# Kernel tuning notes

Measured on AMD Instinct MI355X. Metric: run time of the kernel, lower is better.

## Reference

```python
import jax, jax.numpy as jnp
import numpy as np

KNN_K = 5  # nearest neighbors for local density
PATCH_GRID = 14  # hard-coded p1=p2=14 in rearrange


def _tokens(x):
    # b c (p1 h) (p2 w) -> b (p1 p2) (h w c)
    B, C, H, W = x.shape
    P = PATCH_GRID
    h, w = H // P, W // P
    t = x.reshape(B, C, P, h, P, w).transpose(0, 2, 4, 3, 5, 1)
    return t.reshape(B, P * P, h * w * C)


def _forward(x, len_keep):
    t = _tokens(x)
    B, N, Cf = t.shape
    # pairwise Euclidean distance (torch.cdist) scaled by sqrt(C)
    sq = jnp.sum(t * t, axis=-1)  # [B, N]
    d2 = sq[:, :, None] + sq[:, None, :] - 2.0 * jnp.einsum('bnc,bmc->bnm', t, t)
    dist = jnp.sqrt(jnp.maximum(d2, 0.0)) / jnp.sqrt(jnp.asarray(Cf, dist_dtype := t.dtype))
    # k-NN local density
    neg_vals, _ = jax.lax.top_k(-dist, KNN_K)  # k smallest distances
    dist_nearest = -neg_vals  # [B, N, k]
    density = jnp.exp(-jnp.mean(dist_nearest ** 2, axis=-1))  # [B, N]
    kd = jax.random.fold_in(jax.random.key(1), 0)
    density = density + jax.random.uniform(kd, density.shape, dtype=density.dtype) * 1e-6
    # distance to nearest higher-density point (masked min reduction)
    maskf = (density[:, None, :] > density[:, :, None]).astype(dist.dtype)  # [B, N, N]
    dist_max = jnp.max(dist.reshape(B, -1), axis=-1)[:, None, None]
    dmin = jnp.min(dist * maskf + dist_max * (1.0 - maskf), axis=-1)  # [B, N]
    score = dmin * density
    # pick cluster centers: top len_keep scores
    _, index_down = jax.lax.top_k(score, len_keep)  # [B, K]
    # assign each token to nearest center
    dm_down = jnp.take_along_axis(dist, index_down[:, :, None], axis=1)  # [B, K, N]
    idx_cluster = jnp.argmin(dm_down, axis=1)  # [B, N]
    # force centers to their own cluster id
    idx_cluster = idx_cluster.at[jnp.arange(B)[:, None], index_down].set(
        jnp.arange(len_keep)[None, :])
    # per-cluster counts (every cluster id 0..K-1 present since centers self-assign)
    counts = jnp.sum(jax.nn.one_hot(idx_cluster, len_keep, dtype=jnp.int32), axis=1)  # [B, K]
    idx_counts = jnp.cumsum(counts, axis=-1)
    # pick one representative token per cluster via noisy sort
    kn = jax.random.fold_in(jax.random.key(1), 1)
    noise = jax.random.uniform(kn, (B, N), dtype=dist.dtype)
    order = jnp.argsort(idx_cluster.astype(dist.dtype) + noise, axis=-1)
    idx = jnp.take_along_axis(order, idx_counts - 1, axis=1)  # [B, K]
    return idx


def setup_inputs() -> dict:
    key = jax.random.key(0)
    x = jax.random.normal(key, (256, 3, 224, 224), dtype=jnp.float32)
    return {"x": x, "len_keep": 49}


def reference(x, len_keep):
    return _forward(x, len_keep)
```

## Files before the change

### kernel.cpp

```cpp
#include <hip/hip_runtime.h>
#include <stdint.h>

#define NTOK 196
#define KCL 49
#define IMG 224
#define IMG2 (224*224)
#define KB 64
#define LDP 68

typedef double f64x4 __attribute__((ext_vector_type(4)));

__host__ __device__ __forceinline__ void tf2x32(uint32_t k0, uint32_t k1,
    uint32_t x0, uint32_t x1, uint32_t* o0, uint32_t* o1) {
  uint32_t ks2 = k0 ^ k1 ^ 0x1BD11BDAu;
#define TFR(r) { x0 += x1; x1 = (x1 << r) | (x1 >> (32 - r)); x1 ^= x0; }
  x0 += k0; x1 += k1;
  TFR(13) TFR(15) TFR(26) TFR(6)
  x0 += k1; x1 += ks2 + 1u;
  TFR(17) TFR(29) TFR(16) TFR(24)
  x0 += ks2; x1 += k0 + 2u;
  TFR(13) TFR(15) TFR(26) TFR(6)
  x0 += k0; x1 += k1 + 3u;
  TFR(17) TFR(29) TFR(16) TFR(24)
  x0 += k1; x1 += ks2 + 4u;
  TFR(13) TFR(15) TFR(26) TFR(6)
  x0 += ks2; x1 += k0 + 5u;
#undef TFR
  *o0 = x0; *o1 = x1;
}

__device__ __forceinline__ float jax_uniform(uint32_t k0, uint32_t k1, uint32_t j) {
  uint32_t o0, o1;
  tf2x32(k0, k1, 0u, j, &o0, &o1);
  uint32_t bits = o0 ^ o1;
  return __uint_as_float((bits >> 9) | 0x3f800000u) - 1.0f;
}

__global__ void __launch_bounds__(256) k_sq(const float* __restrict__ x,
                                            double* __restrict__ sq, int B) {
  int wave = blockIdx.x * 4 + (threadIdx.x >> 6);
  int lane = threadIdx.x & 63;
  if (wave >= B * NTOK) return;
  int b = wave / NTOK, n = wave % NTOK;
  int p1 = n / 14, p2 = n % 14;
  const float* xb = x + (size_t)b * 3 * IMG2;
  int rowbase = (p1 * 16) * IMG + p2 * 16;
  double acc = 0.0;
#pragma unroll
  for (int q = 0; q < 12; ++q) {
    int f = lane + q * 64;
    int c = f >> 8, h = (f >> 4) & 15, w = f & 15;
    float v = xb[c * IMG2 + rowbase + h * IMG + w];
    acc += (double)v * (double)v;
  }
#pragma unroll
  for (int off = 32; off; off >>= 1) acc += __shfl_down(acc, off);
  if (lane == 0) sq[wave] = acc;
}

__global__ void __launch_bounds__(256) k_dist_mfma(const float* __restrict__ x,
    const double* __restrict__ sq, double* __restrict__ dist,
    unsigned long long* __restrict__ dmax) {
  int bid = blockIdx.x;
  int xcd = bid & 7;
  int s = bid >> 3;
  int b = xcd + 8 * (s / 28);
  int t = s % 28;
  int ti = 0, rem = t, rl = 7;
  while (rem >= rl) { rem -= rl; rl--; ti++; }
  int tj = ti + rem;
  int n0b = ti * 32, m0b = tj * 32;
  int tid = threadIdx.x;

  __shared__ __align__(16) float As[32][LDP];
  __shared__ __align__(16) float Bs[32][LDP];
  __shared__ int rbN[32], rbM[32];
  __shared__ double prsh[3];
  __shared__ int okf;

  if (tid < 32) {
    int n = n0b + tid; n = n < NTOK ? n : NTOK - 1;
    rbN[tid] = (n / 14) * 16 * IMG + (n % 14) * 16;
  } else if (tid < 64) {
    int m = m0b + (tid - 32); m = m < NTOK ? m : NTOK - 1;
    rbM[tid - 32] = (m / 14) * 16 * IMG + (m % 14) * 16;
  }
  __syncthreads();

  const float* xb = x + (size_t)b * 3 * IMG2;
  int srow = tid >> 3;
  int sfo  = (tid & 7) * 8;
  int rN = rbN[srow], rM = rbM[srow];
  int lane = tid & 63;
  int wid  = tid >> 6;
  int wi = wid >> 1, wj = wid & 1;
  int aq = lane >> 4;
  const float* Ap = &As[0][0];
  const float* Bp = &Bs[0][0];
  int abase = (wi * 16 + (lane & 15)) * LDP + aq;
  int bbase = (wj * 16 + (lane & 15)) * LDP + aq;

#define LOADT(d0,d1,d2,d3,kc) { int f0 = (kc) + sfo;                         \
    int c_ = f0 >> 8, h_ = (f0 >> 4) & 15, w_ = f0 & 15;                     \
    const float* p_ = xb + c_ * IMG2 + h_ * IMG + w_;                        \
    d0 = *(const float4*)(p_ + rN); d1 = *(const float4*)(p_ + rN + 4);      \
    d2 = *(const float4*)(p_ + rM); d3 = *(const float4*)(p_ + rM + 4); }

  f64x4 acc = {0.0, 0.0, 0.0, 0.0};
  f64x4 acc0 = {0.0, 0.0, 0.0, 0.0};
  float4 ca0, ca1, cb0, cb1;
  LOADT(ca0, ca1, cb0, cb1, 0)

#pragma unroll
  for (int tt = 0; tt < 12; ++tt) {
    __syncthreads();
    *(float4*)&As[srow][sfo]     = ca0;
    *(float4*)&As[srow][sfo + 4] = ca1;
    *(float4*)&Bs[srow][sfo]     = cb0;
    *(float4*)&Bs[srow][sfo + 4] = cb1;
    __syncthreads();
    float4 na0, na1, nb0, nb1;
    if (tt < 11) LOADT(na0, na1, nb0, nb1, (tt + 1) * KB)
#pragma unroll
    for (int k = 0; k < KB; k += 4) {
      double av = (double)Ap[abase + k];
      double bv = (double)Bp[bbase + k];
      acc = __builtin_amdgcn_mfma_f64_16x16x4f64(av, bv, acc, 0, 0, 0);
    }
    if (tt == 0) {
      if (wid == 0) {
        double q0 = (double)As[0][lane] * (double)Bs[0][lane];
        double q1 = (double)As[1][lane] * (double)Bs[0][lane];
        double q2 = (double)As[4][lane] * (double)Bs[0][lane];
#pragma unroll
        for (int off = 32; off; off >>= 1) {
          q0 += __shfl_down(q0, off);
          q1 += __shfl_down(q1, off);
          q2 += __shfl_down(q2, off);
        }
        if (lane == 0) { prsh[0] = q0; prsh[1] = q1; prsh[2] = q2; }
      }
      acc0 = acc;
    }
    ca0 = na0; ca1 = na1; cb0 = nb0; cb1 = nb1;
  }
#undef LOADT

  if (tid == 0) {
    double tol = 1e-9 * (1.0 + fabs(prsh[0]));
    int ok0  = fabs(prsh[0] - acc0[0]) <= tol;
    int okP1 = ok0 && (fabs(prsh[1] - acc0[1]) <= tol);
    int okP2 = ok0 && (fabs(prsh[2] - acc0[1]) <= tol);
    okf = okP1 ? 1 : (okP2 ? 2 : 0);
  }
  __syncthreads();
  int mode = okf;

  double (*Dt)[33] = (double(*)[33])(&As[0][0]);

  if (mode) {
#pragma unroll
    for (int i = 0; i < 4; ++i) {
      int lr = (mode == 1) ? (aq * 4 + i) : (aq + 4 * i);
      Dt[wi * 16 + lr][wj * 16 + (lane & 15)] = acc[i];
    }
  } else {
    double s00 = 0, s01 = 0, s10 = 0, s11 = 0;
    int ty2 = tid >> 4, tx2 = tid & 15;
    for (int kc = 0; kc < 768; kc += KB) {
      int f0 = kc + sfo;
      int c_ = f0 >> 8, h_ = (f0 >> 4) & 15, w_ = f0 & 15;
      const float* p_ = xb + c_ * IMG2 + h_ * IMG + w_;
      float4 la0 = *(const float4*)(p_ + rN), la1 = *(const float4*)(p_ + rN + 4);
      float4 lb0 = *(const float4*)(p_ + rM), lb1 = *(const float4*)(p_ + rM + 4);
      __syncthreads();
      *(float4*)&As[srow][sfo]     = la0;
      *(float4*)&As[srow][sfo + 4] = la1;
      *(float4*)&Bs[srow][sfo]     = lb0;
      *(float4*)&Bs[srow][sfo + 4] = lb1;
      __syncthreads();
      for (int j = 0; j < KB; ++j) {
        double a0 = (double)As[ty2][j], a1 = (double)As[ty2 + 16][j];
        double b0 = (double)Bs[tx2][j], b1 = (double)Bs[tx2 + 16][j];
        s00 += a0 * b0; s01 += a0 * b1; s10 += a1 * b0; s11 += a1 * b1;
      }
    }
    __syncthreads();
    Dt[ty2][tx2] = s00;       Dt[ty2][tx2 + 16] = s01;
    Dt[ty2 + 16][tx2] = s10;  Dt[ty2 + 16][tx2 + 16] = s11;
  }
  __syncthreads();

  const double* sqb = sq + b * NTOK;
  const double SQ768 = sqrt(768.0);
  int lr2 = tid >> 3, lc0 = (tid & 7) * 4;
  double dv[4];
  double lmax = 0.0;
#pragma unroll
  for (int j = 0; j < 4; ++j) {
    int n = n0b + lr2, m = m0b + lc0 + j;
    int nn = n < NTOK ? n : NTOK - 1, mm = m < NTOK ? m : NTOK - 1;
    double d2 = sqb[nn] + sqb[mm] - 2.0 * Dt[lr2][lc0 + j];
    double d = sqrt(d2 > 0.0 ? d2 : 0.0) / SQ768;
    dv[j] = d;
    lmax = lmax > d ? lmax : d;
  }
#pragma unroll
  for (int j = 0; j < 4; ++j) Dt[lr2][lc0 + j] = dv[j];
  double* red = (double*)(&Bs[0][0]);
  red[tid] = lmax;
  __syncthreads();
  for (int st = 128; st; st >>= 1) {
    if (tid < st) { double o = red[tid + st]; if (o > red[tid]) red[tid] = o; }
    __syncthreads();
  }
  if (tid == 0) atomicMax(&dmax[b], (unsigned long long)__double_as_longlong(red[0]));

  double* Db = dist + (size_t)b * NTOK * NTOK;
  {
    int n = n0b + lr2, m0 = m0b + lc0;
    if (n < NTOK && m0 < NTOK) {
      if (m0 + 3 < NTOK) {
        f64x4 v = {dv[0], dv[1], dv[2], dv[3]};
        *(f64x4*)(Db + (size_t)n * NTOK + m0) = v;
      } else {
#pragma unroll
        for (int j = 0; j < 4; ++j)
          if (m0 + j < NTOK) Db[(size_t)n * NTOK + m0 + j] = dv[j];
      }
    }
  }
  if (ti != tj) {
    int m = m0b + lr2, n0 = n0b + lc0;
    if (m < NTOK && n0 < NTOK) {
      if (n0 + 3 < NTOK) {
        f64x4 v = {Dt[lc0][lr2], Dt[lc0 + 1][lr2], Dt[lc0 + 2][lr2], Dt[lc0 + 3][lr2]};
        *(f64x4*)(Db + (size_t)m * NTOK + n0) = v;
      } else {
#pragma unroll
        for (int j = 0; j < 4; ++j)
          if (n0 + j < NTOK) Db[(size_t)m * NTOK + n0 + j] = Dt[lc0 + j][lr2];
      }
    }
  }
}

#define INS5(n0_,n1_,n2_,n3_,n4_,v_) {                                        \
  if ((v_) < n4_) { n4_ = (v_);                                               \
    if (n4_ < n3_) { double w_ = n3_; n3_ = n4_; n4_ = w_;                    \
      if (n3_ < n2_) { w_ = n2_; n2_ = n3_; n3_ = w_;                         \
        if (n2_ < n1_) { w_ = n1_; n1_ = n2_; n2_ = w_;                       \
          if (n1_ < n0_) { w_ = n0_; n0_ = n1_; n1_ = w_; } } } } } }

__global__ void __launch_bounds__(512) k_cluster2(const double* __restrict__ dist,
    const unsigned long long* __restrict__ dmax, int* __restrict__ out,
    uint32_t kd0, uint32_t kd1, uint32_t kn0, uint32_t kn1, int B) {
  int b = blockIdx.x;
  int tid = threadIdx.x;
  int lane = tid & 63, wid = tid >> 6;
  const double* Db = dist + (size_t)b * NTOK * NTOK;
  __shared__ double nbsh[NTOK * 5];
  __shared__ double dens[NTOK];
  __shared__ double score[NTOK];
  __shared__ int center[KCL];
  __shared__ short center_of[NTOK];
  __shared__ unsigned long long bkey[KCL];
  double dmaxv = __longlong_as_double((long long)dmax[b]);

  int t = (tid < NTOK) ? tid : tid - NTOK;
  int half = (tid < NTOK) ? 0 : 1;
  bool act = tid < 2 * NTOK;
  int m0 = half ? 98 : 0;

  double pa0 = 1e300, pa1 = 1e300, pa2 = 1e300, pa3 = 1e300, pa4 = 1e300;
  double qa0 = 1e300, qa1 = 1e300, qa2 = 1e300, qa3 = 1e300, qa4 = 1e300;
  if (act) {
    const double* base = Db + t;
    for (int i = 0; i < 49; ++i) {
      double v1 = base[(size_t)(m0 + i) * NTOK];
      double v2 = base[(size_t)(m0 + 49 + i) * NTOK];
      INS5(pa0, pa1, pa2, pa3, pa4, v1)
      INS5(qa0, qa1, qa2, qa3, qa4, v2)
    }
  }
  double nb[5];
  {
    double ax = pa0, a1 = pa1, a2 = pa2, a3 = pa3, a4 = pa4;
    double bx = qa0, b1 = qa1, b2 = qa2, b3 = qa3, b4 = qa4;
#pragma unroll
    for (int p = 0; p < 5; ++p) {
      if (ax <= bx) { nb[p] = ax; ax = a1; a1 = a2; a2 = a3; a3 = a4; a4 = 1e300; }
      else          { nb[p] = bx; bx = b1; b1 = b2; b2 = b3; b3 = b4; b4 = 1e300; }
    }
  }
  if (act && half) {
    nbsh[t * 5 + 0] = nb[0]; nbsh[t * 5 + 1] = nb[1]; nbsh[t * 5 + 2] = nb[2];
    nbsh[t * 5 + 3] = nb[3]; nbsh[t * 5 + 4] = nb[4];
  }
  __syncthreads();
  if (tid < NTOK) {
    double ax = nb[0], a1 = nb[1], a2 = nb[2], a3 = nb[3], a4 = nb[4];
    double bx = nbsh[t * 5 + 0], b1 = nbsh[t * 5 + 1], b2 = nbsh[t * 5 + 2],
           b3 = nbsh[t * 5 + 3], b4 = nbsh[t * 5 + 4];
    double acc = 0.0;
#pragma unroll
    for (int p = 0; p < 5; ++p) {
      double v;
      if (ax <= bx) { v = ax; ax = a1; a1 = a2; a2 = a3; a3 = a4; a4 = 1e300; }
      else          { v = bx; bx = b1; b1 = b2; b2 = b3; b3 = b4; b4 = 1e300; }
      acc += v * v;
    }
    double d = exp(-(acc / 5.0));
    double u = (double)jax_uniform(kd0, kd1, (uint32_t)(b * NTOK + t));
    dens[t] = d + u * 1e-6;
  }
  __syncthreads();

  double vloc = dmaxv;
  if (act) {
    double dn = dens[t];
    const double* base = Db + t;
    double v1 = dmaxv, v2 = dmaxv;
    for (int i = 0; i < 49; ++i) {
      double r1 = base[(size_t)(m0 + i) * NTOK];
      double r2 = base[(size_t)(m0 + 49 + i) * NTOK];
      if (dens[m0 + i] > dn && r1 < v1) v1 = r1;
      if (dens[m0 + 49 + i] > dn && r2 < v2) v2 = r2;
    }
    vloc = v1 < v2 ? v1 : v2;
  }
  __syncthreads();
  if (act && half) nbsh[t] = vloc;
  __syncthreads();
  if (tid < NTOK) {
    double v2 = nbsh[t];
    double v = vloc < v2 ? vloc : v2;
    score[t] = v * dens[t];
  }
  __syncthreads();

  if (wid == 0) {
    double s0 = (lane < NTOK) ? score[lane] : -1e300;
    double s1 = score[lane + 64];
    double s2 = score[lane + 128];
    double s3 = (lane + 192 < NTOK) ? score[lane + 192] : -1e300;
    for (int k = 0; k < KCL; ++k) {
      double mv = s0; int mi = lane;
      if (s1 > mv) { mv = s1; mi = lane + 64; }
      if (s2 > mv) { mv = s2; mi = lane + 128; }
      if (s3 > mv) { mv = s3; mi = lane + 192; }
#pragma unroll
      for (int off = 32; off; off >>= 1) {
        double ov = __shfl_down(mv, off); int oi = __shfl_down(mi, off);
        if (ov > mv || (ov == mv && oi < mi)) { mv = ov; mi = oi; }
      }
      mi = __shfl(mi, 0);
      if (lane == 0) center[k] = mi;
      if (mi == lane) s0 = -1e300;
      else if (mi == lane + 64) s1 = -1e300;
      else if (mi == lane + 128) s2 = -1e300;
      else if (mi == lane + 192) s3 = -1e300;
    }
  }
  __syncthreads();

  if (tid < NTOK) center_of[tid] = -1;
  __syncthreads();
  if (tid < KCL) { center_of[center[tid]] = (short)tid; bkey[tid] = 0ULL; }
  __syncthreads();
  int mycl = 0;
  if (tid < NTOK) {
    double best = 1e300; int bk = 0;
    for (int k = 0; k < KCL; ++k) {
      double d = Db[(size_t)center[k] * NTOK + tid];
      if (d < best) { best = d; bk = k; }
    }
    short co = center_of[tid];
    if (co >= 0) bk = co;
    mycl = bk;
  }
  __syncthreads();

  if (tid < NTOK) {
    float u = jax_uniform(kn0, kn1, (uint32_t)(b * NTOK + tid));
    float keyf = (float)mycl + u;
    unsigned long long key =
        ((unsigned long long)__float_as_uint(keyf) << 8) | (unsigned)tid;
    atomicMax(&bkey[mycl], key);
  }
  __syncthreads();
  if (tid < KCL) out[b * KCL + tid] = (int)(bkey[tid] & 0xFFu);
}

extern "C" void kernel_launch(void* const* d_in, const int* in_sizes, int n_in,
                              void* d_out, int out_size, void* d_ws, size_t ws_size,
                              hipStream_t stream) {
  const float* x = (const float*)d_in[0];
  int B = in_sizes[0] / (3 * IMG2);
  double* dist = (double*)d_ws;
  size_t distBytes = (size_t)B * NTOK * NTOK * sizeof(double);
  double* sq = (double*)((char*)d_ws + distBytes);
  unsigned long long* dmax =
      (unsigned long long*)((char*)sq + (size_t)B * NTOK * sizeof(double));
  int* out = (int*)d_out;

  uint32_t kd0, kd1, kn0, kn1;
  tf2x32(0u, 1u, 0u, 0u, &kd0, &kd1);
  tf2x32(0u, 1u, 0u, 1u, &kn0, &kn1);

  hipMemsetAsync(dmax, 0, B * sizeof(unsigned long long), stream);
  int totalTok = B * NTOK;
  k_sq<<<dim3((totalTok + 3) / 4), dim3(256), 0, stream>>>(x, sq, B);
  k_dist_mfma<<<dim3(8 * 32 * 28), dim3(256), 0, stream>>>(x, sq, dist, dmax);
  k_cluster2<<<dim3(B), dim3(512), 0, stream>>>(dist, dmax, out, kd0, kd1, kn0, kn1, B);
}
```

Measured before the change: 319.1 us.

## Split Gram tiles into diagonal/off-diagonal kernels, derive norms from diagonal, double-buffer LDS

```diff
diff --git a/kernel.cpp b/kernel.cpp
--- a/kernel.cpp
+++ b/kernel.cpp
@@ -36,44 +36,193 @@
   return __uint_as_float((bits >> 9) | 0x3f800000u) - 1.0f;
 }
 
-__global__ void __launch_bounds__(256) k_sq(const float* __restrict__ x,
-                                            double* __restrict__ sq, int B) {
-  int wave = blockIdx.x * 4 + (threadIdx.x >> 6);
-  int lane = threadIdx.x & 63;
-  if (wave >= B * NTOK) return;
-  int b = wave / NTOK, n = wave % NTOK;
-  int p1 = n / 14, p2 = n % 14;
+__global__ void __launch_bounds__(256) k_diag(const float* __restrict__ x,
+    double* __restrict__ sq, double* __restrict__ dist,
+    unsigned long long* __restrict__ dmax) {
+  int bid = blockIdx.x;
+  int xcd = bid & 7;
+  int s = bid >> 3;
+  int b = xcd + 8 * (s / 7);
+  int ti = s % 7;
+  int n0b = ti * 32;
+  int tid = threadIdx.x;
+
+  __shared__ __align__(16) float As0[32][LDP];
+  __shared__ __align__(16) float As1[32][LDP];
+  __shared__ int rbN[32];
+  __shared__ double prsh[3];
+  __shared__ int okf;
+  __shared__ double sqN[32];
+
+  if (tid < 32) {
+    int n = n0b + tid; n = n < NTOK ? n : NTOK - 1;
+    rbN[tid] = (n / 14) * 16 * IMG + (n % 14) * 16;
+  }
+  __syncthreads();
+
   const float* xb = x + (size_t)b * 3 * IMG2;
-  int rowbase = (p1 * 16) * IMG + p2 * 16;
-  double acc = 0.0;
-#pragma unroll
-  for (int q = 0; q < 12; ++q) {
-    int f = lane + q * 64;
-    int c = f >> 8, h = (f >> 4) & 15, w = f & 15;
-    float v = xb[c * IMG2 + rowbase + h * IMG + w];
-    acc += (double)v * (double)v;
-  }
-#pragma unroll
-  for (int off = 32; off; off >>= 1) acc += __shfl_down(acc, off);
-  if (lane == 0) sq[wave] = acc;
+  int srow = tid >> 3;
+  int sfo  = (tid & 7) * 8;
+  int rN = rbN[srow];
+  int lane = tid & 63;
+  int wid  = tid >> 6;
+  int wi = wid >> 1, wj = wid & 1;
+  int aq = lane >> 4;
+  const float* A0 = &As0[0][0];
+  const float* A1 = &As1[0][0];
+  int fragA = (wi * 16 + (lane & 15)) * LDP + aq;
+  int fragB = (wj * 16 + (lane & 15)) * LDP + aq;
+
+#define LOADD(d0,d1,kc) { int f0 = (kc) + sfo;                               \
+    int c_ = f0 >> 8, h_ = (f0 >> 4) & 15, w_ = f0 & 15;                     \
+    const float* p_ = xb + c_ * IMG2 + h_ * IMG + w_;                        \
+    d0 = *(const float4*)(p_ + rN); d1 = *(const float4*)(p_ + rN + 4); }
+
+  f64x4 acc = {0.0, 0.0, 0.0, 0.0};
+  f64x4 acc0 = {0.0, 0.0, 0.0, 0.0};
+  float4 ca0, ca1;
+  LOADD(ca0, ca1, 0)
+  *(float4*)&As0[srow][sfo]     = ca0;
+  *(float4*)&As0[srow][sfo + 4] = ca1;
+  LOADD(ca0, ca1, KB)
+  __syncthreads();
+
+#pragma unroll
+  for (int tt = 0; tt < 12; ++tt) {
+    const float* cur = (tt & 1) ? A1 : A0;
+    float (*nxt)[LDP] = (tt & 1) ? As0 : As1;
+    if (tt < 11) {
+      *(float4*)&nxt[srow][sfo]     = ca0;
+      *(float4*)&nxt[srow][sfo + 4] = ca1;
+    }
+    if (tt < 10) LOADD(ca0, ca1, (tt + 2) * KB)
+#pragma unroll
+    for (int k = 0; k < KB; k += 4) {
+      double av = (double)cur[fragA + k];
+      double bv = (double)cur[fragB + k];
+      acc = __builtin_amdgcn_mfma_f64_16x16x4f64(av, bv, acc, 0, 0, 0);
+    }
+    if (tt == 0) {
+      if (wid == 0) {
+        double q0 = (double)A0[0 * LDP + lane] * (double)A0[0 * LDP + lane];
+        double q1 = (double)A0[1 * LDP + lane] * (double)A0[0 * LDP + lane];
+        double q2 = (double)A0[4 * LDP + lane] * (double)A0[0 * LDP + lane];
+#pragma unroll
+        for (int off = 32; off; off >>= 1) {
+          q0 += __shfl_down(q0, off);
+          q1 += __shfl_down(q1, off);
+          q2 += __shfl_down(q2, off);
+        }
+        if (lane == 0) { prsh[0] = q0; prsh[1] = q1; prsh[2] = q2; }
+      }
+      acc0 = acc;
+    }
+    __syncthreads();
+  }
+#undef LOADD
+
+  if (tid == 0) {
+    double tol = 1e-9 * (1.0 + fabs(prsh[0]));
+    int ok0  = fabs(prsh[0] - acc0[0]) <= tol;
+    int okP1 = ok0 && (fabs(prsh[1] - acc0[1]) <= tol);
+    int okP2 = ok0 && (fabs(prsh[2] - acc0[1]) <= tol);
+    okf = okP1 ? 1 : (okP2 ? 2 : 0);
+  }
+  __syncthreads();
+  int mode = okf;
+
+  double (*Dt)[33] = (double(*)[33])A0;
+
+  if (mode) {
+#pragma unroll
+    for (int i = 0; i < 4; ++i) {
+      int lr = (mode == 1) ? (aq * 4 + i) : (aq + 4 * i);
+      Dt[wi * 16 + lr][wj * 16 + (lane & 15)] = acc[i];
+    }
+  } else {
+    double s00 = 0, s01 = 0, s10 = 0, s11 = 0;
+    int ty2 = tid >> 4, tx2 = tid & 15;
+    for (int kc = 0; kc < 768; kc += KB) {
+      int f0 = kc + sfo;
+      int c_ = f0 >> 8, h_ = (f0 >> 4) & 15, w_ = f0 & 15;
+      const float* p_ = xb + c_ * IMG2 + h_ * IMG + w_;
+      float4 la0 = *(const float4*)(p_ + rN), la1 = *(const float4*)(p_ + rN + 4);
+      __syncthreads();
+      *(float4*)&As0[srow][sfo]     = la0;
+      *(float4*)&As0[srow][sfo + 4] = la1;
+      __syncthreads();
+      for (int j = 0; j < KB; ++j) {
+        double a0 = (double)As0[ty2][j], a1 = (double)As0[ty2 + 16][j];
+        double b0 = (double)As0[tx2][j], b1 = (double)As0[tx2 + 16][j];
+        s00 += a0 * b0; s01 += a0 * b1; s10 += a1 * b0; s11 += a1 * b1;
+      }
+    }
+    __syncthreads();
+    Dt[ty2][tx2] = s00;       Dt[ty2][tx2 + 16] = s01;
+    Dt[ty2 + 16][tx2] = s10;  Dt[ty2 + 16][tx2 + 16] = s11;
+  }
+  __syncthreads();
+
+  if (tid < 32) {
+    double v = Dt[tid][tid];
+    sqN[tid] = v;
+    int n = n0b + tid;
+    if (n < NTOK) sq[b * NTOK + n] = v;
+  }
+  __syncthreads();
+
+  const double SQ768 = sqrt(768.0);
+  int lr2 = tid >> 3, lc0 = (tid & 7) * 4;
+  double dv[4];
+  double lmax = 0.0;
+#pragma unroll
+  for (int j = 0; j < 4; ++j) {
+    double d2 = sqN[lr2] + sqN[lc0 + j] - 2.0 * Dt[lr2][lc0 + j];
+    double d = sqrt(d2 > 0.0 ? d2 : 0.0) / SQ768;
+    dv[j] = d;
+    lmax = lmax > d ? lmax : d;
+  }
+  double* red = (double*)A1;
+  red[tid] = lmax;
+  __syncthreads();
+  for (int st = 128; st; st >>= 1) {
+    if (tid < st) { double o = red[tid + st]; if (o > red[tid]) red[tid] = o; }
+    __syncthreads();
+  }
+  if (tid == 0) atomicMax(&dmax[b], (unsigned long long)__double_as_longlong(red[0]));
+
+  double* Db = dist + (size_t)b * NTOK * NTOK;
+  int n = n0b + lr2, m0 = n0b + lc0;
+  if (n < NTOK && m0 < NTOK) {
+    if (m0 + 3 < NTOK) {
+      f64x4 v = {dv[0], dv[1], dv[2], dv[3]};
+      *(f64x4*)(Db + (size_t)n * NTOK + m0) = v;
+    } else {
+#pragma unroll
+      for (int j = 0; j < 4; ++j)
+        if (m0 + j < NTOK) Db[(size_t)n * NTOK + m0 + j] = dv[j];
+    }
+  }
 }
 
-__global__ void __launch_bounds__(256) k_dist_mfma(const float* __restrict__ x,
+__global__ void __launch_bounds__(256) k_offdiag(const float* __restrict__ x,
     const double* __restrict__ sq, double* __restrict__ dist,
     unsigned long long* __restrict__ dmax) {
   int bid = blockIdx.x;
   int xcd = bid & 7;
   int s = bid >> 3;
-  int b = xcd + 8 * (s / 28);
-  int t = s % 28;
-  int ti = 0, rem = t, rl = 7;
+  int b = xcd + 8 * (s / 21);
+  int t = s % 21;
+  int ti = 0, rem = t, rl = 6;
   while (rem >= rl) { rem -= rl; rl--; ti++; }
-  int tj = ti + rem;
+  int tj = ti + 1 + rem;
   int n0b = ti * 32, m0b = tj * 32;
   int tid = threadIdx.x;
 
-  __shared__ __align__(16) float As[32][LDP];
-  __shared__ __align__(16) float Bs[32][LDP];
+  __shared__ __align__(16) float As0[32][LDP];
+  __shared__ __align__(16) float As1[32][LDP];
+  __shared__ __align__(16) float Bs0[32][LDP];
+  __shared__ __align__(16) float Bs1[32][LDP];
   __shared__ int rbN[32], rbM[32];
   __shared__ double prsh[3];
   __shared__ int okf;
@@ -95,10 +244,12 @@
   int wid  = tid >> 6;
   int wi = wid >> 1, wj = wid & 1;
   int aq = lane >> 4;
-  const float* Ap = &As[0][0];
-  const float* Bp = &Bs[0][0];
-  int abase = (wi * 16 + (lane & 15)) * LDP + aq;
-  int bbase = (wj * 16 + (lane & 15)) * LDP + aq;
+  const float* A0 = &As0[0][0];
+  const float* A1 = &As1[0][0];
+  const float* B0 = &Bs0[0][0];
+  const float* B1 = &Bs1[0][0];
+  int fragA = (wi * 16 + (lane & 15)) * LDP + aq;
+  int fragB = (wj * 16 + (lane & 15)) * LDP + aq;
 
 #define LOADT(d0,d1,d2,d3,kc) { int f0 = (kc) + sfo;                         \
     int c_ = f0 >> 8, h_ = (f0 >> 4) & 15, w_ = f0 & 15;                     \
@@ -110,28 +261,37 @@
   f64x4 acc0 = {0.0, 0.0, 0.0, 0.0};
   float4 ca0, ca1, cb0, cb1;
   LOADT(ca0, ca1, cb0, cb1, 0)
+  *(float4*)&As0[srow][sfo]     = ca0;
+  *(float4*)&As0[srow][sfo + 4] = ca1;
+  *(float4*)&Bs0[srow][sfo]     = cb0;
+  *(float4*)&Bs0[srow][sfo + 4] = cb1;
+  LOADT(ca0, ca1, cb0, cb1, KB)
+  __syncthreads();
 
 #pragma unroll
   for (int tt = 0; tt < 12; ++tt) {
-    __syncthreads();
-    *(float4*)&As[srow][sfo]     = ca0;
-    *(float4*)&As[srow][sfo + 4] = ca1;
-    *(float4*)&Bs[srow][sfo]     = cb0;
-    *(float4*)&Bs[srow][sfo + 4] = cb1;
-    __syncthreads();
-    float4 na0, na1, nb0, nb1;
-    if (tt < 11) LOADT(na0, na1, nb0, nb1, (tt + 1) * KB)
+    const float* curA = (tt & 1) ? A1 : A0;
+    const float* curB = (tt & 1) ? B1 : B0;
+    float (*nxtA)[LDP] = (tt & 1) ? As0 : As1;
+    float (*nxtB)[LDP] = (tt & 1) ? Bs0 : Bs1;
+    if (tt < 11) {
+      *(float4*)&nxtA[srow][sfo]     = ca0;
+      *(float4*)&nxtA[srow][sfo + 4] = ca1;
+      *(float4*)&nxtB[srow][sfo]     = cb0;
+      *(float4*)&nxtB[srow][sfo + 4] = cb1;
+    }
+    if (tt < 10) LOADT(ca0, ca1, cb0, cb1, (tt + 2) * KB)
 #pragma unroll
     for (int k = 0; k < KB; k += 4) {
-      double av = (double)Ap[abase + k];
-      double bv = (double)Bp[bbase + k];
+      double av = (double)curA[fragA + k];
+      double bv = (double)curB[fragB + k];
       acc = __builtin_amdgcn_mfma_f64_16x16x4f64(av, bv, acc, 0, 0, 0);
     }
     if (tt == 0) {
       if (wid == 0) {
-        double q0 = (double)As[0][lane] * (double)Bs[0][lane];
-        double q1 = (double)As[1][lane] * (double)Bs[0][lane];
-        double q2 = (double)As[4][lane] * (double)Bs[0][lane];
+        double q0 = (double)A0[0 * LDP + lane] * (double)B0[0 * LDP + lane];
+        double q1 = (double)A0[1 * LDP + lane] * (double)B0[0 * LDP + lane];
+        double q2 = (double)A0[4 * LDP + lane] * (double)B0[0 * LDP + lane];
 #pragma unroll
         for (int off = 32; off; off >>= 1) {
           q0 += __shfl_down(q0, off);
@@ -142,7 +302,7 @@
       }
       acc0 = acc;
     }
-    ca0 = na0; ca1 = na1; cb0 = nb0; cb1 = nb1;
+    __syncthreads();
   }
 #undef LOADT
 
@@ -156,7 +316,7 @@
   __syncthreads();
   int mode = okf;
 
-  double (*Dt)[33] = (double(*)[33])(&As[0][0]);
+  double (*Dt)[33] = (double(*)[33])A0;
 
   if (mode) {
 #pragma unroll
@@ -174,14 +334,14 @@
       float4 la0 = *(const float4*)(p_ + rN), la1 = *(const float4*)(p_ + rN + 4);
       float4 lb0 = *(const float4*)(p_ + rM), lb1 = *(const float4*)(p_ + rM + 4);
       __syncthreads();
-      *(float4*)&As[srow][sfo]     = la0;
-      *(float4*)&As[srow][sfo + 4] = la1;
-      *(float4*)&Bs[srow][sfo]     = lb0;
-      *(float4*)&Bs[srow][sfo + 4] = lb1;
+      *(float4*)&As0[srow][sfo]     = la0;
+      *(float4*)&As0[srow][sfo + 4] = la1;
+      *(float4*)&Bs0[srow][sfo]     = lb0;
+      *(float4*)&Bs0[srow][sfo + 4] = lb1;
       __syncthreads();
       for (int j = 0; j < KB; ++j) {
-        double a0 = (double)As[ty2][j], a1 = (double)As[ty2 + 16][j];
-        double b0 = (double)Bs[tx2][j], b1 = (double)Bs[tx2 + 16][j];
+        double a0 = (double)As0[ty2][j], a1 = (double)As0[ty2 + 16][j];
+        double b0 = (double)Bs0[tx2][j], b1 = (double)Bs0[tx2 + 16][j];
         s00 += a0 * b0; s01 += a0 * b1; s10 += a1 * b0; s11 += a1 * b1;
       }
     }
@@ -207,7 +367,7 @@
   }
 #pragma unroll
   for (int j = 0; j < 4; ++j) Dt[lr2][lc0 + j] = dv[j];
-  double* red = (double*)(&Bs[0][0]);
+  double* red = (double*)B0;
   red[tid] = lmax;
   __syncthreads();
   for (int st = 128; st; st >>= 1) {
@@ -230,7 +390,7 @@
       }
     }
   }
-  if (ti != tj) {
+  {
     int m = m0b + lr2, n0 = n0b + lc0;
     if (m < NTOK && n0 < NTOK) {
       if (n0 + 3 < NTOK) {
@@ -409,8 +569,7 @@
   tf2x32(0u, 1u, 0u, 1u, &kn0, &kn1);
 
   hipMemsetAsync(dmax, 0, B * sizeof(unsigned long long), stream);
-  int totalTok = B * NTOK;
-  k_sq<<<dim3((totalTok + 3) / 4), dim3(256), 0, stream>>>(x, sq, B);
-  k_dist_mfma<<<dim3(8 * 32 * 28), dim3(256), 0, stream>>>(x, sq, dist, dmax);
+  k_diag<<<dim3(8 * 32 * 7), dim3(256), 0, stream>>>(x, sq, dist, dmax);
+  k_offdiag<<<dim3(8 * 32 * 21), dim3(256), 0, stream>>>(x, sq, dist, dmax);
   k_cluster2<<<dim3(B), dim3(512), 0, stream>>>(dist, dmax, out, kd0, kd1, kn0, kn1, B);
 }
```

Measured after the change: 303.3 us. 4.9% less time.
